# Performance work log

Hardware: AMD Instinct MI355X
Metric: run time of the kernel (lower is better)

Reference implementation:

```python
import jax, jax.numpy as jnp
import numpy as np

# Vim-S config
B, L, D, DEPTH = 16, 197, 384, 24
DI, DS, DTR = 768, 16, 24  # d_inner=2*D, d_state, dt_rank=ceil(D/16)
NUM_CLASSES = 1000
EPS = 1e-5


def setup_inputs() -> dict:
    key = jax.random.key(0)
    ks = jax.random.split(key, 12)
    f = jnp.float32
    rn = lambda k, shp, s=0.02: jax.random.normal(k, shp, f) * s
    inp = {
        'x': jax.random.normal(ks[0], (B, 3, 224, 224), f),
        'patch_w': rn(ks[1], (D, 3, 16, 16)),
        'patch_b': jnp.zeros((D,), f),
        'cls_token': rn(ks[2], (1, 1, D)),
        'pos_embed': rn(ks[3], (1, L, D)),
        'in_proj_w': rn(ks[4], (DEPTH, 2 * DI, D)),
        'conv_w': rn(ks[5], (DEPTH, DI, 1, 4), 0.1),  # depthwise causal conv, d_conv=4
        'conv_b': jnp.zeros((DEPTH, DI), f),
        'x_proj_w': rn(ks[6], (DEPTH, DTR + 2 * DS, DI)),
        'dt_proj_w': rn(ks[7], (DEPTH, DI, DTR), 0.1),
        'dt_proj_b': jnp.full((DEPTH, DI), float(np.log(np.expm1(0.01))), f),
        'A_log': jnp.log(jnp.broadcast_to(jnp.arange(1, DS + 1, dtype=f), (DEPTH, DI, DS))),
        'D_ssm': jnp.ones((DEPTH, DI), f),
        'out_proj_w': rn(ks[8], (DEPTH, D, DI)),
        'norm_w': jnp.ones((DEPTH, D), f),
        'norm_b': jnp.zeros((DEPTH, D), f),
        'normf_w': jnp.ones((D,), f),
        'normf_b': jnp.zeros((D,), f),
        'head_w': rn(ks[9], (NUM_CLASSES, D)),
        'head_b': jnp.zeros((NUM_CLASSES,), f),
    }
    return inp


def _ln(u, w, b):
    mu = u.mean(-1, keepdims=True)
    v = ((u - mu) ** 2).mean(-1, keepdims=True)
    return (u - mu) * jax.lax.rsqrt(v + EPS) * w + b


def _silu(u):
    return u * jax.nn.sigmoid(u)


def _mixer(u, Win, Wc, bc, Wx, Wdt, bdt, Alog, Dp, Wout):
    # u: [B, L, D]
    xz = jnp.einsum('bld,ed->ble', u, Win)            # [B, L, 2*DI]
    xc, z = jnp.split(xz, 2, axis=-1)
    # causal depthwise conv1d (d_conv=4): pad 3 on the left
    xt = jnp.pad(xc.transpose(0, 2, 1), ((0, 0), (0, 0), (3, 0)))
    xt = jax.lax.conv_general_dilated(xt, Wc, (1,), 'VALID',
                                      dimension_numbers=('NCH', 'OIH', 'NCH'),
                                      feature_group_count=DI)
    xc = _silu((xt + bc[None, :, None]).transpose(0, 2, 1))  # [B, L, DI]
    dbl = jnp.einsum('bld,ed->ble', xc, Wx)           # [B, L, DTR+2*DS]
    dt = jax.nn.softplus(jnp.einsum('blr,dr->bld', dbl[..., :DTR], Wdt) + bdt)
    Bm = dbl[..., DTR:DTR + DS]                       # [B, L, DS]
    Cm = dbl[..., DTR + DS:]                          # [B, L, DS]
    A = -jnp.exp(Alog)                                # [DI, DS]
    dA = jnp.exp(jnp.einsum('bld,dn->bldn', dt, A))   # [B, L, DI, DS]
    dBx = jnp.einsum('bld,bln->bldn', dt * xc, Bm)    # [B, L, DI, DS]

    def step(h, inps):
        dA_t, dBx_t, C_t = inps
        h = dA_t * h + dBx_t                          # [B, DI, DS]
        return h, jnp.einsum('bdn,bn->bd', h, C_t)

    h0 = jnp.zeros((u.shape[0], DI, DS), u.dtype)
    _, ys = jax.lax.scan(step, h0, (dA.transpose(1, 0, 2, 3),
                                    dBx.transpose(1, 0, 2, 3),
                                    Cm.transpose(1, 0, 2)))
    y = ys.transpose(1, 0, 2) + xc * Dp               # [B, L, DI]
    y = y * _silu(z)
    return jnp.einsum('ble,de->bld', y, Wout)         # [B, L, D]


def reference(x, patch_w, patch_b, cls_token, pos_embed, in_proj_w, conv_w, conv_b,
              x_proj_w, dt_proj_w, dt_proj_b, A_log, D_ssm, out_proj_w,
              norm_w, norm_b, normf_w, normf_b, head_w, head_b):
    b = x.shape[0]
    # patch embed: Conv2d(3, D, 16, stride 16)
    feat = jax.lax.conv_general_dilated(x, patch_w, (16, 16), 'VALID',
                                        dimension_numbers=('NCHW', 'OIHW', 'NCHW'))
    feat = feat + patch_b[None, :, None, None]
    tokens = feat.reshape(b, D, -1).transpose(0, 2, 1)          # [B, 196, D]
    h = jnp.concatenate([jnp.broadcast_to(cls_token, (b, 1, D)), tokens], axis=1)
    h = h + pos_embed                                           # [B, 197, D]

    def layer(carry, p):
        hid, res = carry
        Win, Wc, bc, Wx, Wdt, bdt, Alog, Dp, Wout, nw, nb = p
        res = res + hid                # (hidden + residual), first layer: residual = hidden
        hid = _mixer(_ln(res, nw, nb), Win, Wc, bc, Wx, Wdt, bdt, Alog, Dp, Wout)
        return (hid, res), None

    (hid, res), _ = jax.lax.scan(layer, (h, jnp.zeros_like(h)),
                                 (in_proj_w, conv_w, conv_b, x_proj_w, dt_proj_w,
                                  dt_proj_b, A_log, D_ssm, out_proj_w, norm_w, norm_b))
    out = _ln(res + hid, normf_w, normf_b)
    return out[:, 0] @ head_w.T + head_b                        # [B, num_classes]
```

## Files before the change

### kernel.cpp

```cpp
#include <hip/hip_runtime.h>
#include <hip/hip_bf16.h>
#include <math.h>

#define BB     16
#define LL     197
#define DD     384
#define DEPTH  24
#define DI     768
#define DSN    16
#define DTR    24
#define NC     1000
#define TT     (BB*LL)
#define NPATCH 196
#define EPSV   1e-5f

#define NCHUNK 12
#define CH     17

typedef __attribute__((ext_vector_type(8))) short short8;
typedef __attribute__((ext_vector_type(4))) short short4v;
typedef __attribute__((ext_vector_type(4))) float f32x4;

__device__ __forceinline__ short f2bf(float f) {
  union { float f; unsigned u; } v; v.f = f;
  unsigned u = v.u + 0x7fffu + ((v.u >> 16) & 1u);
  return (short)(u >> 16);
}

__device__ __forceinline__ void gload16(const short* g, const short* l) {
  __builtin_amdgcn_global_load_lds(
      (const __attribute__((address_space(1))) unsigned int*)g,
      (__attribute__((address_space(3))) unsigned int*)l, 16, 0, 0);
}

__global__ __launch_bounds__(256) void k_cvt4(const float* __restrict__ s0, short* __restrict__ d0, int n0,
                                              const float* __restrict__ s1, short* __restrict__ d1, int n1,
                                              const float* __restrict__ s2, short* __restrict__ d2, int n2,
                                              const float* __restrict__ s3, short* __restrict__ d3, int n3,
                                              int b0, int b1, int b2) {
  int blk = blockIdx.x;
  const float* src; short* dst; int n; int lb;
  if (blk < b0)      { src = s0; dst = d0; n = n0; lb = blk; }
  else if (blk < b1) { src = s1; dst = d1; n = n1; lb = blk - b0; }
  else if (blk < b2) { src = s2; dst = d2; n = n2; lb = blk - b1; }
  else               { src = s3; dst = d3; n = n3; lb = blk - b2; }
  int i = (lb * 256 + threadIdx.x) * 4;
  if (i + 3 < n) {
    float4 v = *(const float4*)&src[i];
    short4v o = {f2bf(v.x), f2bf(v.y), f2bf(v.z), f2bf(v.w)};
    *(short4v*)&dst[i] = o;
  } else {
    for (int j = 0; i + j < n && j < 4; j++) dst[i + j] = f2bf(src[i + j]);
  }
}

__global__ __launch_bounds__(256) void k_init(const float* __restrict__ cls,
                                              const float* __restrict__ pos,
                                              float* __restrict__ res) {
  int i = blockIdx.x * 256 + threadIdx.x;
  if (i < BB * DD) {
    int b = i / DD, d = i % DD;
    res[(size_t)(b * LL) * DD + d] = cls[d] + pos[d];
  }
}

__global__ __launch_bounds__(256) void k_patch(const float* __restrict__ x,
                                               const float* __restrict__ pw,
                                               const float* __restrict__ pb,
                                               const float* __restrict__ pos,
                                               float* __restrict__ res) {
  __shared__ short sA[64 * 40];
  __shared__ short sB[64 * 40];
  const int tid = threadIdx.x;
  const int m0 = blockIdx.x * 64, n0 = blockIdx.y * 64;
  const int srow = tid >> 2;
  const int skq = (tid & 3) * 8;
  const int lane = tid & 63, w = tid >> 6;
  const int wm = (w >> 1) * 32, wn = (w & 1) * 32;
  const int fr = lane & 15;
  const int fk = (lane >> 4) * 8;
  f32x4 acc[2][2] = {};
  const int m = m0 + srow;
  const int b = m / NPATCH;
  const int p = m % NPATCH;
  const int ph = p / 14, pwi = p % 14;
  const float* Wrow = pw + (size_t)(n0 + srow) * 768 + skq;
  for (int k0 = 0; k0 < 768; k0 += 32) {
    int k = k0 + skq;
    int c = k >> 8, rr = (k >> 4) & 15, kw = k & 15;
    const float* xrow = &x[(size_t)(((b * 3 + c) * 224) + (ph * 16 + rr)) * 224 +
                           (pwi * 16 + kw)];
    float4 a0 = *(const float4*)&xrow[0];
    float4 a1 = *(const float4*)&xrow[4];
    float4 b0 = *(const float4*)&Wrow[k0];
    float4 b1 = *(const float4*)&Wrow[k0 + 4];
    short8 av = {f2bf(a0.x), f2bf(a0.y), f2bf(a0.z), f2bf(a0.w),
                 f2bf(a1.x), f2bf(a1.y), f2bf(a1.z), f2bf(a1.w)};
    short8 bv = {f2bf(b0.x), f2bf(b0.y), f2bf(b0.z), f2bf(b0.w),
                 f2bf(b1.x), f2bf(b1.y), f2bf(b1.z), f2bf(b1.w)};
    *(short8*)&sA[srow * 40 + skq] = av;
    *(short8*)&sB[srow * 40 + skq] = bv;
    __syncthreads();
    short8 af0 = *(const short8*)&sA[(wm + fr) * 40 + fk];
    short8 af1 = *(const short8*)&sA[(wm + 16 + fr) * 40 + fk];
    short8 bf0 = *(const short8*)&sB[(wn + fr) * 40 + fk];
    short8 bf1 = *(const short8*)&sB[(wn + 16 + fr) * 40 + fk];
    acc[0][0] = __builtin_amdgcn_mfma_f32_16x16x32_bf16(af0, bf0, acc[0][0], 0, 0, 0);
    acc[0][1] = __builtin_amdgcn_mfma_f32_16x16x32_bf16(af0, bf1, acc[0][1], 0, 0, 0);
    acc[1][0] = __builtin_amdgcn_mfma_f32_16x16x32_bf16(af1, bf0, acc[1][0], 0, 0, 0);
    acc[1][1] = __builtin_amdgcn_mfma_f32_16x16x32_bf16(af1, bf1, acc[1][1], 0, 0, 0);
    __syncthreads();
  }
#pragma unroll
  for (int i = 0; i < 2; i++)
#pragma unroll
    for (int j = 0; j < 2; j++)
#pragma unroll
      for (int q = 0; q < 4; q++) {
        int mm = m0 + wm + i * 16 + (lane >> 4) * 4 + q;
        int nn = n0 + wn + j * 16 + (lane & 15);
        int b2 = mm / NPATCH, pp = mm % NPATCH;
        int tok = b2 * LL + 1 + pp;
        res[(size_t)tok * DD + nn] = acc[i][j][q] + pb[nn] + pos[(size_t)(1 + pp) * DD + nn];
      }
}

__global__ __launch_bounds__(256) void k_gemm128(const short* __restrict__ A, int lda,
                                                 const short* __restrict__ W, int ldb,
                                                 float* __restrict__ C, int ldc,
                                                 int M, int N, int K) {
  __shared__ short sA[128 * 32];
  __shared__ short sB[128 * 32];
  const int tid = threadIdx.x;
  const int lane = tid & 63, w = tid >> 6;
  const int m0 = blockIdx.x * 128, n0 = blockIdx.y * 128;
  const int wm = (w >> 1) * 64, wn = (w & 1) * 64;
  const int fr = lane & 15;
  const int fk = (lane >> 4) * 8;
  const int q0 = w * 2, q1 = w * 2 + 1;
  const int sr0 = q0 * 16 + (lane >> 2);
  const int sr1 = q1 * 16 + (lane >> 2);
  const int scol = (lane & 3) * 8;
  f32x4 acc[4][4] = {};
  const short* Ab0 = A + (size_t)(m0 + sr0) * lda + scol;
  const short* Ab1 = A + (size_t)(m0 + sr1) * lda + scol;
  const short* Bb0 = W + (size_t)(n0 + sr0) * ldb + scol;
  const short* Bb1 = W + (size_t)(n0 + sr1) * ldb + scol;
  for (int k0 = 0; k0 < K; k0 += 32) {
    gload16(Ab0 + k0, &sA[q0 * 512]);
    gload16(Ab1 + k0, &sA[q1 * 512]);
    gload16(Bb0 + k0, &sB[q0 * 512]);
    gload16(Bb1 + k0, &sB[q1 * 512]);
    __syncthreads();
    short8 af[4], bf[4];
#pragma unroll
    for (int i = 0; i < 4; i++) {
      af[i] = *(const short8*)&sA[(wm + i * 16 + fr) * 32 + fk];
      bf[i] = *(const short8*)&sB[(wn + i * 16 + fr) * 32 + fk];
    }
#pragma unroll
    for (int i = 0; i < 4; i++)
#pragma unroll
      for (int j = 0; j < 4; j++)
        acc[i][j] = __builtin_amdgcn_mfma_f32_16x16x32_bf16(af[i], bf[j], acc[i][j], 0, 0, 0);
    __syncthreads();
  }
#pragma unroll
  for (int i = 0; i < 4; i++)
#pragma unroll
    for (int j = 0; j < 4; j++)
#pragma unroll
      for (int q = 0; q < 4; q++) {
        int mm = m0 + wm + i * 16 + (lane >> 4) * 4 + q;
        int nn = n0 + wn + j * 16 + fr;
        if (mm < M) C[(size_t)mm * ldc + nn] = acc[i][j][q];
      }
}

__global__ __launch_bounds__(256) void k_gemm64(const short* __restrict__ A, int lda,
                                                const short* __restrict__ W, int ldb,
                                                float* __restrict__ C, int ldc,
                                                int M, int N, int K) {
  __shared__ short sA[64 * 32];
  __shared__ short sB[64 * 32];
  const int tid = threadIdx.x;
  const int lane = tid & 63, w = tid >> 6;
  const int m0 = blockIdx.x * 64, n0 = blockIdx.y * 64;
  const int wm = (w >> 1) * 32, wn = (w & 1) * 32;
  const int fr = lane & 15;
  const int fk = (lane >> 4) * 8;
  const int srow = w * 16 + (lane >> 2);
  const int scol = (lane & 3) * 8;
  f32x4 acc[2][2] = {};
  const short* Ab = A + (size_t)(m0 + srow) * lda + scol;
  const short* Bb = W + (size_t)(n0 + srow) * ldb + scol;
  for (int k0 = 0; k0 < K; k0 += 32) {
    gload16(Ab + k0, &sA[w * 512]);
    gload16(Bb + k0, &sB[w * 512]);
    __syncthreads();
    short8 af0 = *(const short8*)&sA[(wm + fr) * 32 + fk];
    short8 af1 = *(const short8*)&sA[(wm + 16 + fr) * 32 + fk];
    short8 bf0 = *(const short8*)&sB[(wn + fr) * 32 + fk];
    short8 bf1 = *(const short8*)&sB[(wn + 16 + fr) * 32 + fk];
    acc[0][0] = __builtin_amdgcn_mfma_f32_16x16x32_bf16(af0, bf0, acc[0][0], 0, 0, 0);
    acc[0][1] = __builtin_amdgcn_mfma_f32_16x16x32_bf16(af0, bf1, acc[0][1], 0, 0, 0);
    acc[1][0] = __builtin_amdgcn_mfma_f32_16x16x32_bf16(af1, bf0, acc[1][0], 0, 0, 0);
    acc[1][1] = __builtin_amdgcn_mfma_f32_16x16x32_bf16(af1, bf1, acc[1][1], 0, 0, 0);
    __syncthreads();
  }
#pragma unroll
  for (int i = 0; i < 2; i++)
#pragma unroll
    for (int j = 0; j < 2; j++)
#pragma unroll
      for (int q = 0; q < 4; q++) {
        int mm = m0 + wm + i * 16 + (lane >> 4) * 4 + q;
        int nn = n0 + wn + j * 16 + fr;
        if (mm < M) C[(size_t)mm * ldc + nn] += acc[i][j][q];
      }
}

__global__ __launch_bounds__(256) void k_conv(const float* __restrict__ xz,
                                              const float* __restrict__ wc,
                                              const float* __restrict__ bc,
                                              float* __restrict__ xc,
                                              short* __restrict__ xcbf) {
  int i = blockIdx.x * 256 + threadIdx.x;
  if (i >= TT * (DI / 4)) return;
  int eg = i % (DI / 4);
  int t = i / (DI / 4);
  int e = eg * 4;
  int b = t / LL, l = t % LL;
  const float* base = xz + (size_t)(b * LL) * (2 * DI) + e;
  float4 w0 = *(const float4*)&wc[(e + 0) * 4];
  float4 w1 = *(const float4*)&wc[(e + 1) * 4];
  float4 w2 = *(const float4*)&wc[(e + 2) * 4];
  float4 w3 = *(const float4*)&wc[(e + 3) * 4];
  float4 acc = *(const float4*)&bc[e];
  if (l >= 3) {
    float4 xv = *(const float4*)&base[(size_t)(l - 3) * (2 * DI)];
    acc.x += xv.x * w0.x; acc.y += xv.y * w1.x; acc.z += xv.z * w2.x; acc.w += xv.w * w3.x;
  }
  if (l >= 2) {
    float4 xv = *(const float4*)&base[(size_t)(l - 2) * (2 * DI)];
    acc.x += xv.x * w0.y; acc.y += xv.y * w1.y; acc.z += xv.z * w2.y; acc.w += xv.w * w3.y;
  }
  if (l >= 1) {
    float4 xv = *(const float4*)&base[(size_t)(l - 1) * (2 * DI)];
    acc.x += xv.x * w0.z; acc.y += xv.y * w1.z; acc.z += xv.z * w2.z; acc.w += xv.w * w3.z;
  }
  {
    float4 xv = *(const float4*)&base[(size_t)l * (2 * DI)];
    acc.x += xv.x * w0.w; acc.y += xv.y * w1.w; acc.z += xv.z * w2.w; acc.w += xv.w * w3.w;
  }
  acc.x = acc.x / (1.f + __expf(-acc.x));
  acc.y = acc.y / (1.f + __expf(-acc.y));
  acc.z = acc.z / (1.f + __expf(-acc.z));
  acc.w = acc.w / (1.f + __expf(-acc.w));
  *(float4*)&xc[(size_t)t * DI + e] = acc;
  short4v ov = {f2bf(acc.x), f2bf(acc.y), f2bf(acc.z), f2bf(acc.w)};
  *(short4v*)&xcbf[(size_t)t * DI + e] = ov;
}

__global__ __launch_bounds__(256, 1) void k_xd(const short* __restrict__ xcbf,
                                               const short* __restrict__ wx,
                                               const short* __restrict__ wdt,
                                               const float* __restrict__ dbias,
                                               float* __restrict__ dbl,
                                               float* __restrict__ dtb) {
  __shared__ short sDT[16 * 40];
  const int tid = threadIdx.x;
  const int t0 = blockIdx.x * 16;
  const int lane = tid & 63, w = tid >> 6;
  const int fr = lane & 15;
  const int fk = (lane >> 4) * 8;
  f32x4 acc0 = {}, acc1 = {};
  const short* Arow = xcbf + (size_t)(t0 + fr) * DI + fk;
  const short* Wrow = wx + (size_t)(w * 16 + fr) * DI + fk;
#pragma unroll
  for (int k0 = 0; k0 < DI; k0 += 64) {
    short8 af0 = *(const short8*)&Arow[k0];
    short8 bf0 = *(const short8*)&Wrow[k0];
    short8 af1 = *(const short8*)&Arow[k0 + 32];
    short8 bf1 = *(const short8*)&Wrow[k0 + 32];
    acc0 = __builtin_amdgcn_mfma_f32_16x16x32_bf16(af0, bf0, acc0, 0, 0, 0);
    acc1 = __builtin_amdgcn_mfma_f32_16x16x32_bf16(af1, bf1, acc1, 0, 0, 0);
  }
  f32x4 accx = acc0 + acc1;
  {
    int nn = w * 16 + fr;
#pragma unroll
    for (int q = 0; q < 4; q++) {
      int row = (lane >> 4) * 4 + q;
      int t = t0 + row;
      if (nn >= DTR && nn < 56) dbl[(size_t)t * 56 + nn] = accx[q];
      if (w < 2) sDT[row * 40 + nn] = (nn < DTR) ? f2bf(accx[q]) : (short)0;
    }
  }
  __syncthreads();
  short8 adt = *(const short8*)&sDT[fr * 40 + fk];
  const int g = lane >> 4;
#pragma unroll
  for (int jj = 0; jj < 12; jj++) {
    int j = w * 12 + jj;
    short8 bdt = short8{0, 0, 0, 0, 0, 0, 0, 0};
    if (g < 3) bdt = *(const short8*)&wdt[(size_t)(j * 16 + fr) * DTR + g * 8];
    f32x4 p = {};
    p = __builtin_amdgcn_mfma_f32_16x16x32_bf16(adt, bdt, p, 0, 0, 0);
    int nc = j * 16 + fr;
    float bv = dbias[nc];
#pragma unroll
    for (int q = 0; q < 4; q++) {
      int t = t0 + (lane >> 4) * 4 + q;
      float v = p[q] + bv;
      v = (v > 20.f) ? v : __logf(1.f + __expf(v));
      dtb[(size_t)t * DI + nc] = v;
    }
  }
}

__global__ __launch_bounds__(768) void k_scan(const float* __restrict__ dt,
                                              const float* __restrict__ xc,
                                              const float* __restrict__ xz,
                                              const float* __restrict__ dbl,
                                              const float* __restrict__ Alog,
                                              const float* __restrict__ Dp,
                                              short* __restrict__ ybf) {
  __shared__ float carry[NCHUNK][32][2][17];
  const int tid = threadIdx.x;
  const int c  = tid >> 6;
  const int nh = (tid >> 5) & 1;
  const int el = tid & 31;
  const int e  = blockIdx.x * 32 + el;
  const int b  = blockIdx.y;
  float4 al0 = *(const float4*)&Alog[(size_t)e * DSN + nh * 8];
  float4 al1 = *(const float4*)&Alog[(size_t)e * DSN + nh * 8 + 4];
  float negA[8] = {-__expf(al0.x), -__expf(al0.y), -__expf(al0.z), -__expf(al0.w),
                   -__expf(al1.x), -__expf(al1.y), -__expf(al1.z), -__expf(al1.w)};
  const int l0 = c * CH;
  const int l1 = (l0 + CH < LL) ? (l0 + CH) : LL;
  const size_t tbase = (size_t)b * LL;
  if (c < NCHUNK - 1) {
    float h[8] = {};
    float asum = 0.f;
    for (int l = l0; l < l1; l++) {
      size_t t = tbase + l;
      float dtv = dt[t * DI + e];
      float xcv = xc[t * DI + e];
      float4 B0 = *(const float4*)&dbl[t * 56 + DTR + nh * 8];
      float4 B1 = *(const float4*)&dbl[t * 56 + DTR + nh * 8 + 4];
      float dx = dtv * xcv;
      float Bv[8] = {B0.x, B0.y, B0.z, B0.w, B1.x, B1.y, B1.z, B1.w};
#pragma unroll
      for (int j = 0; j < 8; j++)
        h[j] = __expf(dtv * negA[j]) * h[j] + dx * Bv[j];
      asum += dtv;
    }
#pragma unroll
    for (int j = 0; j < 8; j++) {
      carry[c][el][nh][j]     = __expf(asum * negA[j]);
      carry[c][el][nh][8 + j] = h[j];
    }
  }
  __syncthreads();
  float h[8] = {};
  for (int cp = 0; cp < c; cp++) {
#pragma unroll
    for (int j = 0; j < 8; j++)
      h[j] = carry[cp][el][nh][j] * h[j] + carry[cp][el][nh][8 + j];
  }
  const float dpv = Dp[e];
  for (int l = l0; l < l1; l++) {
    size_t t = tbase + l;
    float dtv = dt[t * DI + e];
    float xcv = xc[t * DI + e];
    float zv = xz[t * (2 * DI) + DI + e];
    float4 B0 = *(const float4*)&dbl[t * 56 + DTR + nh * 8];
    float4 B1 = *(const float4*)&dbl[t * 56 + DTR + nh * 8 + 4];
    float4 C0 = *(const float4*)&dbl[t * 56 + DTR + DSN + nh * 8];
    float4 C1 = *(const float4*)&dbl[t * 56 + DTR + DSN + nh * 8 + 4];
    float dx = dtv * xcv;
    float Bv[8] = {B0.x, B0.y, B0.z, B0.w, B1.x, B1.y, B1.z, B1.w};
    float Cv[8] = {C0.x, C0.y, C0.z, C0.w, C1.x, C1.y, C1.z, C1.w};
    float acc = 0.f;
#pragma unroll
    for (int j = 0; j < 8; j++) {
      h[j] = __expf(dtv * negA[j]) * h[j] + dx * Bv[j];
      acc += h[j] * Cv[j];
    }
    acc += __shfl_xor(acc, 32);
    if (nh == 0) {
      float sz = zv * (1.f / (1.f + __expf(-zv)));
      ybf[t * DI + e] = f2bf((acc + xcv * dpv) * sz);
    }
  }
}

__global__ __launch_bounds__(256) void k_ln(const float* __restrict__ res,
                                            short* __restrict__ u,
                                            const float* __restrict__ nw,
                                            const float* __restrict__ nb) {
  const int lane = threadIdx.x & 63;
  const int t = blockIdx.x * 4 + (threadIdx.x >> 6);
  float r[6];
  float s = 0.f, sq = 0.f;
#pragma unroll
  for (int j = 0; j < 6; j++) {
    int d = lane + j * 64;
    float v = res[(size_t)t * DD + d];
    r[j] = v;
    s += v; sq += v * v;
  }
#pragma unroll
  for (int o = 32; o > 0; o >>= 1) { s += __shfl_xor(s, o); sq += __shfl_xor(sq, o); }
  float mu = s * (1.f / 384.f);
  float var = sq * (1.f / 384.f) - mu * mu;
  float rs = rsqrtf(var + EPSV);
#pragma unroll
  for (int j = 0; j < 6; j++) {
    int d = lane + j * 64;
    u[(size_t)t * DD + d] = f2bf((r[j] - mu) * rs * nw[d] + nb[d]);
  }
}

__global__ __launch_bounds__(256) void k_final(const float* __restrict__ res,
                                               const float* __restrict__ nfw,
                                               const float* __restrict__ nfb,
                                               const float* __restrict__ hw,
                                               const float* __restrict__ hb,
                                               float* __restrict__ out) {
  const int b = blockIdx.y;
  const int c0 = blockIdx.x * 125;
  const int tid = threadIdx.x;
  __shared__ float u0[DD];
  __shared__ float ls[4], lq[4];
  const size_t t0 = (size_t)b * LL * DD;
  float v0 = res[t0 + tid];
  float v1 = (tid < 128) ? res[t0 + 256 + tid] : 0.f;
  float s = v0 + v1, sq = v0 * v0 + v1 * v1;
#pragma unroll
  for (int o = 32; o > 0; o >>= 1) { s += __shfl_xor(s, o); sq += __shfl_xor(sq, o); }
  if ((tid & 63) == 0) { ls[tid >> 6] = s; lq[tid >> 6] = sq; }
  __syncthreads();
  float st = ls[0] + ls[1] + ls[2] + ls[3];
  float qt = lq[0] + lq[1] + lq[2] + lq[3];
  float mu = st * (1.f / 384.f);
  float var = qt * (1.f / 384.f) - mu * mu;
  float rs = rsqrtf(var + EPSV);
  u0[tid] = (v0 - mu) * rs * nfw[tid] + nfb[tid];
  if (tid < 128) u0[256 + tid] = (v1 - mu) * rs * nfw[256 + tid] + nfb[256 + tid];
  __syncthreads();
  int c = c0 + tid;
  if (tid < 125 && c < NC) {
    float acc = hb[c];
    const float* wrow = hw + (size_t)c * DD;
    for (int d = 0; d < DD; d += 4) {
      float4 w4 = *(const float4*)&wrow[d];
      acc += u0[d] * w4.x + u0[d + 1] * w4.y + u0[d + 2] * w4.z + u0[d + 3] * w4.w;
    }
    out[(size_t)b * NC + c] = acc;
  }
}

extern "C" void kernel_launch(void* const* d_in, const int* in_sizes, int n_in,
                              void* d_out, int out_size, void* d_ws, size_t ws_size,
                              hipStream_t stream) {
  const float* x       = (const float*)d_in[0];
  const float* patch_w = (const float*)d_in[1];
  const float* patch_b = (const float*)d_in[2];
  const float* cls     = (const float*)d_in[3];
  const float* pos     = (const float*)d_in[4];
  const float* in_proj = (const float*)d_in[5];
  const float* conv_w  = (const float*)d_in[6];
  const float* conv_b  = (const float*)d_in[7];
  const float* x_proj  = (const float*)d_in[8];
  const float* dt_w    = (const float*)d_in[9];
  const float* dt_b    = (const float*)d_in[10];
  const float* A_log   = (const float*)d_in[11];
  const float* D_ssm   = (const float*)d_in[12];
  const float* out_w   = (const float*)d_in[13];
  const float* norm_w  = (const float*)d_in[14];
  const float* norm_b  = (const float*)d_in[15];
  const float* normf_w = (const float*)d_in[16];
  const float* normf_b = (const float*)d_in[17];
  const float* head_w  = (const float*)d_in[18];
  const float* head_b  = (const float*)d_in[19];
  float* out = (float*)d_out;

  float* ws = (float*)d_ws;
  float* res = ws;  ws += (size_t)TT * DD;
  float* u_r = ws;  ws += (size_t)TT * DD;
  float* xzb = ws;  ws += (size_t)TT * 2 * DI;
  float* xcb = ws;  ws += (size_t)TT * DI;
  float* dbl = ws;  ws += (size_t)TT * 56;
  float* dtb = ws;  ws += (size_t)TT * DI;
  float* ybf_r = ws; ws += (size_t)TT * DI / 2;
  float* xcbf_r = ws; ws += (size_t)TT * DI / 2;
  short* winbf  = (short*)ws; ws += (size_t)DEPTH * 2 * DI * DD / 2;
  short* woutbf = (short*)ws; ws += (size_t)DEPTH * DD * DI / 2;
  short* wxbf   = (short*)ws; ws += (size_t)DEPTH * 56 * DI / 2;
  short* wdtbf  = (short*)ws; ws += (size_t)DEPTH * DI * DTR / 2;

  short* u    = (short*)u_r;
  short* ybf  = (short*)ybf_r;
  short* xcbf = (short*)xcbf_r;

  {
    int n1 = DEPTH * 2 * DI * DD;
    int n2 = DEPTH * DD * DI;
    int n3 = DEPTH * 56 * DI;
    int n4 = DEPTH * DI * DTR;
    int g1 = (n1 / 4 + 255) / 256;
    int g2 = (n2 / 4 + 255) / 256;
    int g3 = (n3 / 4 + 255) / 256;
    int g4 = (n4 / 4 + 255) / 256;
    k_cvt4<<<g1 + g2 + g3 + g4, 256, 0, stream>>>(
        in_proj, winbf, n1, out_w, woutbf, n2, x_proj, wxbf, n3, dt_w, wdtbf, n4,
        g1, g1 + g2, g1 + g2 + g3);
  }

  k_init<<<(BB * DD + 255) / 256, 256, 0, stream>>>(cls, pos, res);
  k_patch<<<dim3(49, 6), 256, 0, stream>>>(x, patch_w, patch_b, pos, res);

  for (int layer = 0; layer < DEPTH; layer++) {
    k_ln<<<TT / 4, 256, 0, stream>>>(res, u, norm_w + layer * DD,
                                     norm_b + layer * DD);
    k_gemm128<<<dim3(25, 12), 256, 0, stream>>>(
        u, DD, winbf + (size_t)layer * 2 * DI * DD, DD, xzb, 2 * DI, TT, 2 * DI, DD);
    k_conv<<<(TT * (DI / 4) + 255) / 256, 256, 0, stream>>>(
        xzb, conv_w + layer * DI * 4, conv_b + layer * DI, xcb, xcbf);
    k_xd<<<dim3(TT / 16), 256, 0, stream>>>(
        xcbf, wxbf + (size_t)layer * 56 * DI, wdtbf + (size_t)layer * DI * DTR,
        dt_b + layer * DI, dbl, dtb);
    k_scan<<<dim3(DI / 32, BB), 768, 0, stream>>>(
        dtb, xcb, xzb, dbl, A_log + (size_t)layer * DI * DSN,
        D_ssm + layer * DI, ybf);
    k_gemm64<<<dim3(50, 6), 256, 0, stream>>>(
        ybf, DI, woutbf + (size_t)layer * DD * DI, DI, res, DD, TT, DD, DI);
  }

  k_final<<<dim3(8, BB), 256, 0, stream>>>(res, normf_w, normf_b, head_w, head_b, out);
}
```

Baseline: 2.480 ms.

## Fuse causal conv+SiLU into x_proj/dt_proj kernel via LDS-staged xz rows

Merges the depthwise causal conv + SiLU kernel into the x_proj/dt_proj MFMA kernel. Each 16-token block stages 19 rows of xz (with 3-row halo), conv weights and bias into LDS via global_load_lds, computes the conv, and keeps the bf16 activations in LDS for the x_proj MFMA. This drops one launch per layer and the global bf16 xc round trip. In exchange it uses about 80KB of LDS per block, which limits occupancy, and adds redundant halo loads.

After: 2.490 ms. About the same (+0.4%).

```diff
diff --git a/kernel.cpp b/kernel.cpp
--- a/kernel.cpp
+++ b/kernel.cpp
@@ -16,6 +16,7 @@
 
 #define NCHUNK 12
 #define CH     17
+#define XZROWS 19
 
 typedef __attribute__((ext_vector_type(8))) short short8;
 typedef __attribute__((ext_vector_type(4))) short short4v;
@@ -28,6 +29,11 @@
 }
 
 __device__ __forceinline__ void gload16(const short* g, const short* l) {
+  __builtin_amdgcn_global_load_lds(
+      (const __attribute__((address_space(1))) unsigned int*)g,
+      (__attribute__((address_space(3))) unsigned int*)l, 16, 0, 0);
+}
+__device__ __forceinline__ void gload16f(const float* g, const float* l) {
   __builtin_amdgcn_global_load_lds(
       (const __attribute__((address_space(1))) unsigned int*)g,
       (__attribute__((address_space(3))) unsigned int*)l, 16, 0, 0);
@@ -220,81 +226,100 @@
       }
 }
 
-__global__ __launch_bounds__(256) void k_conv(const float* __restrict__ xz,
-                                              const float* __restrict__ wc,
-                                              const float* __restrict__ bc,
-                                              float* __restrict__ xc,
-                                              short* __restrict__ xcbf) {
-  int i = blockIdx.x * 256 + threadIdx.x;
-  if (i >= TT * (DI / 4)) return;
-  int eg = i % (DI / 4);
-  int t = i / (DI / 4);
-  int e = eg * 4;
-  int b = t / LL, l = t % LL;
-  const float* base = xz + (size_t)(b * LL) * (2 * DI) + e;
-  float4 w0 = *(const float4*)&wc[(e + 0) * 4];
-  float4 w1 = *(const float4*)&wc[(e + 1) * 4];
-  float4 w2 = *(const float4*)&wc[(e + 2) * 4];
-  float4 w3 = *(const float4*)&wc[(e + 3) * 4];
-  float4 acc = *(const float4*)&bc[e];
-  if (l >= 3) {
-    float4 xv = *(const float4*)&base[(size_t)(l - 3) * (2 * DI)];
-    acc.x += xv.x * w0.x; acc.y += xv.y * w1.x; acc.z += xv.z * w2.x; acc.w += xv.w * w3.x;
-  }
-  if (l >= 2) {
-    float4 xv = *(const float4*)&base[(size_t)(l - 2) * (2 * DI)];
-    acc.x += xv.x * w0.y; acc.y += xv.y * w1.y; acc.z += xv.z * w2.y; acc.w += xv.w * w3.y;
-  }
-  if (l >= 1) {
-    float4 xv = *(const float4*)&base[(size_t)(l - 1) * (2 * DI)];
-    acc.x += xv.x * w0.z; acc.y += xv.y * w1.z; acc.z += xv.z * w2.z; acc.w += xv.w * w3.z;
-  }
-  {
-    float4 xv = *(const float4*)&base[(size_t)l * (2 * DI)];
-    acc.x += xv.x * w0.w; acc.y += xv.y * w1.w; acc.z += xv.z * w2.w; acc.w += xv.w * w3.w;
-  }
-  acc.x = acc.x / (1.f + __expf(-acc.x));
-  acc.y = acc.y / (1.f + __expf(-acc.y));
-  acc.z = acc.z / (1.f + __expf(-acc.z));
-  acc.w = acc.w / (1.f + __expf(-acc.w));
-  *(float4*)&xc[(size_t)t * DI + e] = acc;
-  short4v ov = {f2bf(acc.x), f2bf(acc.y), f2bf(acc.z), f2bf(acc.w)};
-  *(short4v*)&xcbf[(size_t)t * DI + e] = ov;
-}
-
-__global__ __launch_bounds__(256, 1) void k_xd(const short* __restrict__ xcbf,
-                                               const short* __restrict__ wx,
-                                               const short* __restrict__ wdt,
-                                               const float* __restrict__ dbias,
-                                               float* __restrict__ dbl,
-                                               float* __restrict__ dtb) {
+__global__ __launch_bounds__(256, 1) void k_cxd3(const float* __restrict__ xz,
+                                                 const float* __restrict__ wc,
+                                                 const float* __restrict__ bc,
+                                                 const short* __restrict__ wx,
+                                                 const short* __restrict__ wdt,
+                                                 const float* __restrict__ dbias,
+                                                 float* __restrict__ xc,
+                                                 float* __restrict__ dbl,
+                                                 float* __restrict__ dtb) {
+  __shared__ float sXZ[XZROWS * 768];
+  __shared__ float sWC[768 * 4];
+  __shared__ float sBC[768];
+  __shared__ short sXC[16 * 776];
   __shared__ short sDT[16 * 40];
   const int tid = threadIdx.x;
   const int t0 = blockIdx.x * 16;
-  const int lane = tid & 63, w = tid >> 6;
+  const int lane = tid & 63, wv = tid >> 6;
+  for (int r = wv; r < XZROWS; r += 4) {
+    int srow = t0 - 3 + r; if (srow < 0) srow = 0;
+    const float* src = xz + (size_t)srow * (2 * DI);
+#pragma unroll
+    for (int s = 0; s < 3; s++)
+      gload16f(src + s * 256 + lane * 4, &sXZ[r * 768 + s * 256]);
+  }
+#pragma unroll
+  for (int s = 0; s < 3; s++) {
+    int off = (wv * 3 + s) * 256;
+    gload16f(wc + off + lane * 4, &sWC[off]);
+  }
+  if (wv < 3) {
+    int off = wv * 256;
+    gload16f(bc + off + lane * 4, &sBC[off]);
+  }
+  __syncthreads();
+#pragma unroll
+  for (int it = 0; it < 12; it++) {
+    int g = tid + it * 256;
+    int tl = g / 192, eg = g % 192;
+    int e = eg * 4;
+    int t = t0 + tl;
+    int l = t % LL;
+    const float* baseL = &sXZ[(tl + 3) * 768 + e];
+    float4 w0 = *(const float4*)&sWC[(e + 0) * 4];
+    float4 w1 = *(const float4*)&sWC[(e + 1) * 4];
+    float4 w2 = *(const float4*)&sWC[(e + 2) * 4];
+    float4 w3 = *(const float4*)&sWC[(e + 3) * 4];
+    float4 acc = *(const float4*)&sBC[e];
+    if (l >= 3) {
+      float4 xv = *(const float4*)&baseL[-3 * 768];
+      acc.x += xv.x * w0.x; acc.y += xv.y * w1.x; acc.z += xv.z * w2.x; acc.w += xv.w * w3.x;
+    }
+    if (l >= 2) {
+      float4 xv = *(const float4*)&baseL[-2 * 768];
+      acc.x += xv.x * w0.y; acc.y += xv.y * w1.y; acc.z += xv.z * w2.y; acc.w += xv.w * w3.y;
+    }
+    if (l >= 1) {
+      float4 xv = *(const float4*)&baseL[-768];
+      acc.x += xv.x * w0.z; acc.y += xv.y * w1.z; acc.z += xv.z * w2.z; acc.w += xv.w * w3.z;
+    }
+    {
+      float4 xv = *(const float4*)&baseL[0];
+      acc.x += xv.x * w0.w; acc.y += xv.y * w1.w; acc.z += xv.z * w2.w; acc.w += xv.w * w3.w;
+    }
+    acc.x = acc.x / (1.f + __expf(-acc.x));
+    acc.y = acc.y / (1.f + __expf(-acc.y));
+    acc.z = acc.z / (1.f + __expf(-acc.z));
+    acc.w = acc.w / (1.f + __expf(-acc.w));
+    *(float4*)&xc[(size_t)t * DI + e] = acc;
+    short4v ov = {f2bf(acc.x), f2bf(acc.y), f2bf(acc.z), f2bf(acc.w)};
+    *(short4v*)&sXC[tl * 776 + e] = ov;
+  }
+  __syncthreads();
   const int fr = lane & 15;
   const int fk = (lane >> 4) * 8;
   f32x4 acc0 = {}, acc1 = {};
-  const short* Arow = xcbf + (size_t)(t0 + fr) * DI + fk;
-  const short* Wrow = wx + (size_t)(w * 16 + fr) * DI + fk;
+  const short* Wrow = wx + (size_t)(wv * 16 + fr) * DI + fk;
 #pragma unroll
   for (int k0 = 0; k0 < DI; k0 += 64) {
-    short8 af0 = *(const short8*)&Arow[k0];
+    short8 af0 = *(const short8*)&sXC[fr * 776 + k0 + fk];
     short8 bf0 = *(const short8*)&Wrow[k0];
-    short8 af1 = *(const short8*)&Arow[k0 + 32];
+    short8 af1 = *(const short8*)&sXC[fr * 776 + k0 + 32 + fk];
     short8 bf1 = *(const short8*)&Wrow[k0 + 32];
     acc0 = __builtin_amdgcn_mfma_f32_16x16x32_bf16(af0, bf0, acc0, 0, 0, 0);
     acc1 = __builtin_amdgcn_mfma_f32_16x16x32_bf16(af1, bf1, acc1, 0, 0, 0);
   }
   f32x4 accx = acc0 + acc1;
   {
-    int nn = w * 16 + fr;
+    int nn = wv * 16 + fr;
 #pragma unroll
     for (int q = 0; q < 4; q++) {
       int row = (lane >> 4) * 4 + q;
       int t = t0 + row;
       if (nn >= DTR && nn < 56) dbl[(size_t)t * 56 + nn] = accx[q];
-      if (w < 2) sDT[row * 40 + nn] = (nn < DTR) ? f2bf(accx[q]) : (short)0;
+      if (wv < 2) sDT[row * 40 + nn] = (nn < DTR) ? f2bf(accx[q]) : (short)0;
     }
   }
   __syncthreads();
@@ -302,7 +327,7 @@
   const int g = lane >> 4;
 #pragma unroll
   for (int jj = 0; jj < 12; jj++) {
-    int j = w * 12 + jj;
+    int j = wv * 12 + jj;
     short8 bdt = short8{0, 0, 0, 0, 0, 0, 0, 0};
     if (g < 3) bdt = *(const short8*)&wdt[(size_t)(j * 16 + fr) * DTR + g * 8];
     f32x4 p = {};
@@ -495,7 +520,6 @@
   float* dbl = ws;  ws += (size_t)TT * 56;
   float* dtb = ws;  ws += (size_t)TT * DI;
   float* ybf_r = ws; ws += (size_t)TT * DI / 2;
-  float* xcbf_r = ws; ws += (size_t)TT * DI / 2;
   short* winbf  = (short*)ws; ws += (size_t)DEPTH * 2 * DI * DD / 2;
   short* woutbf = (short*)ws; ws += (size_t)DEPTH * DD * DI / 2;
   short* wxbf   = (short*)ws; ws += (size_t)DEPTH * 56 * DI / 2;
@@ -503,7 +527,6 @@
 
   short* u    = (short*)u_r;
   short* ybf  = (short*)ybf_r;
-  short* xcbf = (short*)xcbf_r;
 
   {
     int n1 = DEPTH * 2 * DI * DD;
@@ -527,11 +550,10 @@
                                      norm_b + layer * DD);
     k_gemm128<<<dim3(25, 12), 256, 0, stream>>>(
         u, DD, winbf + (size_t)layer * 2 * DI * DD, DD, xzb, 2 * DI, TT, 2 * DI, DD);
-    k_conv<<<(TT * (DI / 4) + 255) / 256, 256, 0, stream>>>(
-        xzb, conv_w + layer * DI * 4, conv_b + layer * DI, xcb, xcbf);
-    k_xd<<<dim3(TT / 16), 256, 0, stream>>>(
-        xcbf, wxbf + (size_t)layer * 56 * DI, wdtbf + (size_t)layer * DI * DTR,
-        dt_b + layer * DI, dbl, dtb);
+    k_cxd3<<<dim3(TT / 16), 256, 0, stream>>>(
+        xzb, conv_w + layer * DI * 4, conv_b + layer * DI,
+        wxbf + (size_t)layer * 56 * DI, wdtbf + (size_t)layer * DI * DTR,
+        dt_b + layer * DI, xcb, dbl, dtb);
     k_scan<<<dim3(DI / 32, BB), 768, 0, stream>>>(
         dtb, xcb, xzb, dbl, A_log + (size_t)layer * DI * DSN,
         D_ssm + layer * DI, ybf);
```
